# Kernel optimization log

Measured on AMD Instinct MI355X. Metric: run time of the kernel, lower is better.

Reference implementation:

```python
import jax, jax.numpy as jnp
import numpy as np

SQ, B, H = 2048, 1, 4096
NP, HN, MQG = 32, 128, 2          # query heads, head_dim, kv groups
ROT = HN // 2                      # rotary dim = 64 (partial rotary)
NORM = float(np.sqrt(HN))


def apply_rope(x, rope):
    # x: [sq, b, nh, hn]; rope: [sq, 1, ROT//2, 2] (cos, sin)
    sq, b, nh, hn = x.shape
    rot = rope.shape[-2] * 2
    xr, xp = x[..., :rot], x[..., rot:]
    xs = xr.reshape(sq, b, nh, rot // 2, 2)
    rc = rope[:sq].reshape(sq, -1, 1, rot // 2, 2)
    o0 = xs[..., 0] * rc[..., 0] - xs[..., 1] * rc[..., 1]
    o1 = xs[..., 1] * rc[..., 0] + xs[..., 0] * rc[..., 1]
    out = jnp.stack([o0, o1], -1).reshape(sq, b, nh, rot)
    return jnp.concatenate([out, xp], axis=-1)


def setup_inputs() -> dict:
    key = jax.random.key(0)
    k0, k1, k2, k3 = jax.random.split(key, 4)
    qkv_dim = NP * HN + 2 * MQG * HN  # 4608
    hidden_states = jax.random.normal(k0, (SQ, B, H), jnp.float32) * 0.02
    Wqkv = jax.random.normal(k1, (qkv_dim, H), jnp.float32) * 0.02
    bqkv = jax.random.normal(k2, (qkv_dim,), jnp.float32) * 0.02
    Wdense = jax.random.normal(k3, (H, NP * HN), jnp.float32) * 0.02
    # rope cache [sq, 1, ROT//2, 2]
    pos = jnp.arange(SQ, dtype=jnp.float32)
    inv = 1.0 / (10000.0 ** (jnp.arange(0, ROT, 2, dtype=jnp.float32) / ROT))
    ang = pos[:, None] * inv[None, :]
    rotary_pos_emb = jnp.stack([jnp.cos(ang), jnp.sin(ang)], -1)[:, None, :, :]
    # additive causal mask [b, 1, sq, sq]
    causal = jnp.tril(jnp.ones((SQ, SQ), bool))
    attention_mask = jnp.broadcast_to(
        jnp.where(causal, 0.0, -1e9).astype(jnp.float32), (B, 1, SQ, SQ))
    return dict(hidden_states=hidden_states, Wqkv=Wqkv, bqkv=bqkv,
                Wdense=Wdense, rotary_pos_emb=rotary_pos_emb,
                attention_mask=attention_mask)


def reference(hidden_states, Wqkv, bqkv, Wdense, rotary_pos_emb, attention_mask):
    sq, b, _ = hidden_states.shape
    mixed = hidden_states @ Wqkv.T + bqkv            # [sq, b, 4608]
    qd, kvd = NP * HN, MQG * HN
    q = mixed[..., :qd].reshape(sq, b, NP, HN)
    k = mixed[..., qd:qd + kvd].reshape(sq, b, MQG, HN)
    v = mixed[..., qd + kvd:].reshape(sq, b, MQG, HN)
    q = apply_rope(q, rotary_pos_emb)
    k = apply_rope(k, rotary_pos_emb)
    # -> [b, heads, sq, hn]
    q = q.transpose(1, 2, 0, 3)
    k = k.transpose(1, 2, 0, 3)
    v = v.transpose(1, 2, 0, 3)
    # MQA grouping: q [b, g, n_rep, sq, hn]; kv kept at [b, g, sq, hn]
    n_rep = NP // MQG
    qg = q.reshape(b, MQG, n_rep, sq, HN)
    scores = jnp.einsum('bgrqd,bgkd->bgrqk', qg, k) / NORM
    scores = scores + attention_mask[:, None]        # [b,1,1,sq,sq] broadcast
    probs = jax.nn.softmax(scores.astype(jnp.float32), axis=-1).astype(q.dtype)
    ctx = jnp.einsum('bgrqk,bgkd->bgrqd', probs, v)  # [b, g, n_rep, sq, hn]
    ctx = ctx.reshape(b, NP, sq, HN).transpose(0, 2, 1, 3).reshape(b, sq, NP * HN)
    out = ctx @ Wdense.T                             # [b, sq, H]
    return out
```

## Files before the change

kernel.cpp:

```cpp
#include <hip/hip_runtime.h>
#include <stdint.h>

#define SQL 2048
#define HID 4096
#define NHEADS 32
#define HDSZ 128
#define QKVD 4608
#define QDIM 4096

typedef unsigned short u16;
typedef __attribute__((ext_vector_type(8))) short short8;
typedef __attribute__((ext_vector_type(4))) float f32x4;

#define AS1(p) ((__attribute__((address_space(1))) void*)(p))
#define AS3(p) ((__attribute__((address_space(3))) void*)(p))

__device__ __forceinline__ float bf2f(u16 u) {
  return __uint_as_float(((uint32_t)u) << 16);
}
__device__ __forceinline__ u16 f2bf(float f) {
  uint32_t x = __float_as_uint(f);
  x += 0x7fffu + ((x >> 16) & 1u);
  return (u16)(x >> 16);
}

__global__ void k_cvt(const float* __restrict__ in, u16* __restrict__ out, int n8) {
  int i = blockIdx.x * blockDim.x + threadIdx.x;
  int stride = gridDim.x * blockDim.x;
  for (; i < n8; i += stride) {
    const float4* p = reinterpret_cast<const float4*>(in) + (size_t)i * 2;
    float4 a = p[0], b = p[1];
    short8 o;
    o[0] = (short)f2bf(a.x); o[1] = (short)f2bf(a.y);
    o[2] = (short)f2bf(a.z); o[3] = (short)f2bf(a.w);
    o[4] = (short)f2bf(b.x); o[5] = (short)f2bf(b.y);
    o[6] = (short)f2bf(b.z); o[7] = (short)f2bf(b.w);
    reinterpret_cast<short8*>(out)[i] = o;
  }
}

template<int MODE>
__global__ __launch_bounds__(256, 2)
void k_gemm(const u16* __restrict__ A, const u16* __restrict__ B,
            const float* __restrict__ bias,
            u16* __restrict__ qbuf, u16* __restrict__ kbuf, u16* __restrict__ vtbuf,
            float* __restrict__ outf)
{
  __shared__ __align__(16) u16 ldsA[128 * 64];
  __shared__ __align__(16) u16 ldsB[128 * 64];
  const int tid = threadIdx.x;
  const int wid = tid >> 6, lane = tid & 63;
  const int l15 = lane & 15, lg = lane >> 4;
  const int m0 = blockIdx.y * 128, n0 = blockIdx.x * 128;
  const int wr = wid >> 1, wc = wid & 1;

  f32x4 acc[4][4] = {};

  const int srow = lane >> 3;
  const int skb  = (((lane & 7) ^ srow) << 4);
  const size_t rowbytes = (size_t)HID * 2;

  for (int t = 0; t < HID / 64; ++t) {
    __syncthreads();
    const char* Ab = (const char*)A + (size_t)m0 * rowbytes + (size_t)t * 128;
    const char* Bb = (const char*)B + (size_t)n0 * rowbytes + (size_t)t * 128;
#pragma unroll
    for (int i = 0; i < 4; ++i) {
      int seg = i * 4 + wid;
      int row = seg * 8 + srow;
      __builtin_amdgcn_global_load_lds(AS1(Ab + (size_t)row * rowbytes + skb),
                                       AS3(ldsA + seg * 512), 16, 0, 0);
      __builtin_amdgcn_global_load_lds(AS1(Bb + (size_t)row * rowbytes + skb),
                                       AS3(ldsB + seg * 512), 16, 0, 0);
    }
    __syncthreads();
#pragma unroll
    for (int kc = 0; kc < 2; ++kc) {
      short8 af[4], bfr[4];
#pragma unroll
      for (int mi = 0; mi < 4; ++mi) {
        int row = wr * 64 + mi * 16 + l15;
        int kb = (kc * 64 + lg * 16) ^ ((row & 7) << 4);
        af[mi] = *reinterpret_cast<const short8*>((const char*)ldsA + row * 128 + kb);
      }
#pragma unroll
      for (int ni = 0; ni < 4; ++ni) {
        int row = wc * 64 + ni * 16 + l15;
        int kb = (kc * 64 + lg * 16) ^ ((row & 7) << 4);
        bfr[ni] = *reinterpret_cast<const short8*>((const char*)ldsB + row * 128 + kb);
      }
#pragma unroll
      for (int mi = 0; mi < 4; ++mi)
#pragma unroll
        for (int ni = 0; ni < 4; ++ni)
          acc[mi][ni] = __builtin_amdgcn_mfma_f32_16x16x32_bf16(af[mi], bfr[ni], acc[mi][ni], 0, 0, 0);
    }
  }

#pragma unroll
  for (int mi = 0; mi < 4; ++mi) {
#pragma unroll
    for (int ni = 0; ni < 4; ++ni) {
      int row0 = m0 + wr * 64 + mi * 16 + lg * 4;
      int col  = n0 + wc * 64 + ni * 16 + l15;
      if (MODE == 0) {
        float bv = bias[col];
#pragma unroll
        for (int j = 0; j < 4; ++j) {
          float v = acc[mi][ni][j] + bv;
          int r = row0 + j;
          if (col < QDIM) {
            v *= 0.08838834764831845f;
            int hh = col >> 7, d = col & 127;
            qbuf[((size_t)hh * SQL + r) * HDSZ + d] = f2bf(v);
          } else if (col < QDIM + 256) {
            int c2 = col - QDIM; int g = c2 >> 7, d = c2 & 127;
            kbuf[((size_t)g * SQL + r) * HDSZ + d] = f2bf(v);
          } else {
            int c2 = col - QDIM - 256; int g = c2 >> 7, d = c2 & 127;
            vtbuf[((size_t)g * HDSZ + d) * SQL + r] = f2bf(v);
          }
        }
      } else {
#pragma unroll
        for (int j = 0; j < 4; ++j)
          outf[(size_t)(row0 + j) * QDIM + col] = acc[mi][ni][j];
      }
    }
  }
}

__global__ void k_rope(u16* __restrict__ qbuf, u16* __restrict__ kbuf,
                       const float* __restrict__ rope) {
  int idx = blockIdx.x * blockDim.x + threadIdx.x;
  if (idx >= SQL * 34 * 32) return;
  int p = idx & 31;
  int hh = (idx >> 5) % 34;
  int s = idx / (34 * 32);
  float c  = rope[s * 64 + p * 2 + 0];
  float sn = rope[s * 64 + p * 2 + 1];
  u16* base = (hh < 32) ? (qbuf + ((size_t)hh * SQL + s) * HDSZ)
                        : (kbuf + ((size_t)(hh - 32) * SQL + s) * HDSZ);
  u16* pp = base + 2 * p;
  uint32_t packed = *reinterpret_cast<uint32_t*>(pp);
  float x0 = bf2f((u16)(packed & 0xffff));
  float x1 = bf2f((u16)(packed >> 16));
  float o0 = x0 * c - x1 * sn;
  float o1 = x1 * c + x0 * sn;
  *reinterpret_cast<uint32_t*>(pp) = (uint32_t)f2bf(o0) | ((uint32_t)f2bf(o1) << 16);
}

__global__ __launch_bounds__(512, 2)
void k_attn(const u16* __restrict__ qbuf, const u16* __restrict__ kbuf,
            const u16* __restrict__ vtbuf, u16* __restrict__ ctx)
{
  __shared__ __align__(16) u16 KL[2][64 * 128];
  __shared__ __align__(16) u16 VL[2][128 * 64];
  __shared__ uint32_t plw[8][32][36];
  const int tid = threadIdx.x;
  const int wid = tid >> 6, lane = tid & 63;
  const int l15 = lane & 15, lg = lane >> 4;
  const int h = blockIdx.x;
  const int g = h >> 4;
  const int bq = blockIdx.y;
  const int q0 = wid * 256 + bq * 32;
  const int ext = q0 + 32;
  const int NT = (1824 + 32 * bq + 63) >> 6;

  const int cA = tid, cB = tid + 512;
  const int krA = cA >> 4, kiA = (cA & 15) ^ (krA & 7);
  const int krB = cB >> 4, kiB = (cB & 15) ^ (krB & 7);
  const int vrA = cA >> 3, viA = (cA & 7) ^ (vrA & 7);
  const int vrB = cB >> 3, viB = (cB & 7) ^ (vrB & 7);
  const char* kg = (const char*)(kbuf + (size_t)g * SQL * HDSZ);
  const char* vg = (const char*)(vtbuf + (size_t)g * HDSZ * SQL);

#define STAGE(t, b)                                                             \
  do {                                                                          \
    int j0s = (t) * 64;                                                         \
    __builtin_amdgcn_global_load_lds(AS1(kg + (size_t)(j0s + krA) * 256 + (kiA << 4)), \
                                     AS3((char*)KL[b] + cA * 16), 16, 0, 0);    \
    __builtin_amdgcn_global_load_lds(AS1(kg + (size_t)(j0s + krB) * 256 + (kiB << 4)), \
                                     AS3((char*)KL[b] + cB * 16), 16, 0, 0);    \
    __builtin_amdgcn_global_load_lds(AS1(vg + (size_t)vrA * (SQL * 2) + j0s * 2 + (viA << 4)), \
                                     AS3((char*)VL[b] + cA * 16), 16, 0, 0);    \
    __builtin_amdgcn_global_load_lds(AS1(vg + (size_t)vrB * (SQL * 2) + j0s * 2 + (viB << 4)), \
                                     AS3((char*)VL[b] + cB * 16), 16, 0, 0);    \
  } while (0)

  short8 aq[2][4];
#pragma unroll
  for (int rt = 0; rt < 2; ++rt) {
    const u16* qp = qbuf + ((size_t)h * SQL + q0 + rt * 16 + l15) * HDSZ + lg * 8;
#pragma unroll
    for (int kc = 0; kc < 4; ++kc)
      aq[rt][kc] = *reinterpret_cast<const short8*>(qp + kc * 32);
  }
  f32x4 o[2][8] = {};
  float mrow[2], lrow[2];
#pragma unroll
  for (int rt = 0; rt < 2; ++rt) { mrow[rt] = -__builtin_inff(); lrow[rt] = 0.f; }

  STAGE(0, 0);
  __syncthreads();

  for (int i = 0; i < NT; ++i) {
    const int cur = i & 1;
    if (i + 1 < NT) STAGE(i + 1, cur ^ 1);

    const int j0 = i * 64;
    if (j0 < ext) {
      const char* kb0 = (const char*)KL[cur];
      const char* vb0 = (const char*)VL[cur];
      const int swz = (l15 & 7) << 4;

      f32x4 st[2][4] = {};
#pragma unroll
      for (int kc = 0; kc < 4; ++kc) {
        short8 bk4[4];
#pragma unroll
        for (int kt = 0; kt < 4; ++kt) {
          int r = 16 * kt + l15;
          bk4[kt] = *reinterpret_cast<const short8*>(
              kb0 + r * 256 + ((kc * 64 + lg * 16) ^ swz));
        }
        __builtin_amdgcn_s_setprio(1);
#pragma unroll
        for (int rt = 0; rt < 2; ++rt)
#pragma unroll
          for (int kt = 0; kt < 4; ++kt)
            st[rt][kt] = __builtin_amdgcn_mfma_f32_16x16x32_bf16(bk4[kt], aq[rt][kc], st[rt][kt], 0, 0, 0);
        __builtin_amdgcn_s_setprio(0);
      }

      const bool domask = (j0 + 63 > q0);
#pragma unroll
      for (int rt = 0; rt < 2; ++rt) {
        const int q = q0 + rt * 16 + l15;
        float p[4][4];
#pragma unroll
        for (int kt = 0; kt < 4; ++kt)
#pragma unroll
          for (int j = 0; j < 4; ++j) {
            float v = st[rt][kt][j];
            if (domask) {
              int kvi = j0 + kt * 16 + lg * 4 + j;
              v = (kvi > q) ? -1e30f : v;
            }
            p[kt][j] = v;
          }
        float rm = fmaxf(fmaxf(fmaxf(p[0][0], p[0][1]), fmaxf(p[0][2], p[0][3])),
                         fmaxf(fmaxf(p[1][0], p[1][1]), fmaxf(p[1][2], p[1][3])));
        rm = fmaxf(rm, fmaxf(fmaxf(fmaxf(p[2][0], p[2][1]), fmaxf(p[2][2], p[2][3])),
                             fmaxf(fmaxf(p[3][0], p[3][1]), fmaxf(p[3][2], p[3][3]))));
        rm = fmaxf(rm, __shfl_xor(rm, 16));
        rm = fmaxf(rm, __shfl_xor(rm, 32));
        if (!__all(rm <= mrow[rt] + 8.0f)) {
          float mn = fmaxf(mrow[rt], rm);
          float a = __expf(mrow[rt] - mn);
          mrow[rt] = mn;
          lrow[rt] *= a;
          float ar[4];
#pragma unroll
          for (int j = 0; j < 4; ++j) ar[j] = __shfl(a, lg * 4 + j);
#pragma unroll
          for (int df = 0; df < 8; ++df) {
            o[rt][df][0] *= ar[0]; o[rt][df][1] *= ar[1];
            o[rt][df][2] *= ar[2]; o[rt][df][3] *= ar[3];
          }
        }
        float ps = 0.f;
#pragma unroll
        for (int kt = 0; kt < 4; ++kt)
#pragma unroll
          for (int j = 0; j < 4; ++j) {
            p[kt][j] = __expf(p[kt][j] - mrow[rt]);
            ps += p[kt][j];
          }
        ps += __shfl_xor(ps, 16);
        ps += __shfl_xor(ps, 32);
        lrow[rt] += ps;
#pragma unroll
        for (int kt = 0; kt < 4; ++kt)
#pragma unroll
          for (int u = 0; u < 2; ++u) {
            uint32_t W;
            asm("v_cvt_pk_bf16_f32 %0, %1, %2"
                : "=v"(W) : "v"(p[kt][2 * u]), "v"(p[kt][2 * u + 1]));
            plw[wid][rt * 16 + l15][8 * kt + 2 * lg + u] = W;
          }
      }
      asm volatile("s_waitcnt lgkmcnt(0)" ::: "memory");

      short8 ap[2][2];
#pragma unroll
      for (int rt = 0; rt < 2; ++rt)
#pragma unroll
        for (int kc2 = 0; kc2 < 2; ++kc2)
          ap[rt][kc2] = *reinterpret_cast<const short8*>(&plw[wid][rt * 16 + l15][16 * kc2 + 4 * lg]);

      __builtin_amdgcn_s_setprio(1);
#pragma unroll
      for (int df = 0; df < 8; ++df) {
        short8 bv0, bv1;
        int rv = l15 + 16 * df;
#pragma unroll
        for (int kc2 = 0; kc2 < 2; ++kc2) {
          short8 bvv = *reinterpret_cast<const short8*>(
              vb0 + rv * 128 + ((kc2 * 64 + lg * 16) ^ swz));
          if (kc2 == 0) bv0 = bvv; else bv1 = bvv;
        }
#pragma unroll
        for (int rt = 0; rt < 2; ++rt) {
          f32x4 t = o[rt][df];
          t = __builtin_amdgcn_mfma_f32_16x16x32_bf16(ap[rt][0], bv0, t, 0, 0, 0);
          t = __builtin_amdgcn_mfma_f32_16x16x32_bf16(ap[rt][1], bv1, t, 0, 0, 0);
          o[rt][df] = t;
        }
      }
      __builtin_amdgcn_s_setprio(0);
    }
    __syncthreads();
  }

#pragma unroll
  for (int rt = 0; rt < 2; ++rt) {
    float linv[4];
#pragma unroll
    for (int j = 0; j < 4; ++j) linv[j] = 1.0f / __shfl(lrow[rt], lg * 4 + j);
#pragma unroll
    for (int j = 0; j < 4; ++j) {
      int row = q0 + rt * 16 + lg * 4 + j;
      u16* cp = ctx + (size_t)row * QDIM + h * HDSZ;
#pragma unroll
      for (int df = 0; df < 8; ++df)
        cp[df * 16 + l15] = f2bf(o[rt][df][j] * linv[j]);
    }
  }
#undef STAGE
}


extern "C" void kernel_launch(void* const* d_in, const int* in_sizes, int n_in,
                              void* d_out, int out_size, void* d_ws, size_t ws_size,
                              hipStream_t stream) {
  const float* hs     = (const float*)d_in[0];
  const float* wqkv   = (const float*)d_in[1];
  const float* bqkv   = (const float*)d_in[2];
  const float* wdense = (const float*)d_in[3];
  const float* rope   = (const float*)d_in[4];
  char* ws = (char*)d_ws;
  u16* hid_b = (u16*)(ws + 0);
  u16* w_b   = (u16*)(ws + 16777216);
  u16* qb    = (u16*)(ws + 54525952);
  u16* kb    = (u16*)(ws + 71303168);
  u16* vtb   = (u16*)(ws + 72351744);
  u16* ctx   = hid_b;
  float* outf = (float*)d_out;

  k_cvt<<<2048, 256, 0, stream>>>(hs,   hid_b, SQL * HID / 8);
  k_cvt<<<2048, 256, 0, stream>>>(wqkv, w_b,   QKVD * HID / 8);
  k_gemm<0><<<dim3(QKVD / 128, SQL / 128), 256, 0, stream>>>(
      hid_b, w_b, bqkv, qb, kb, vtb, nullptr);
  k_rope<<<(SQL * 34 * 32) / 256, 256, 0, stream>>>(qb, kb, rope);
  k_cvt<<<2048, 256, 0, stream>>>(wdense, w_b, QDIM * HID / 8);
  k_attn<<<dim3(NHEADS, 8), 512, 0, stream>>>(qb, kb, vtb, ctx);
  k_gemm<1><<<dim3(QDIM / 128, SQL / 128), 256, 0, stream>>>(
      ctx, w_b, nullptr, nullptr, nullptr, nullptr, outf);
}
```

Before: 302.3 us.

## Double-buffer GEMM LDS tiles with async prefetch, XCD block swizzle, MFMA priority

Turns the QKV/dense GEMM main loop into a two-stage pipeline. The next K tile is loaded into a second LDS buffer with global_load_lds while MFMAs run on the current one, and synchronisation uses explicit vmcnt waits with raw barriers. Workgroup IDs are remapped so that consecutive tiles land on the same XCD, which improves L2 reuse. s_setprio is raised around the MFMA block. LDS use doubles to 64KB per block, which may reduce occupancy from the two blocks per CU requested in launch bounds.

```diff
diff --git a/kernel.cpp b/kernel.cpp
--- a/kernel.cpp
+++ b/kernel.cpp
@@ -46,12 +46,18 @@
             u16* __restrict__ qbuf, u16* __restrict__ kbuf, u16* __restrict__ vtbuf,
             float* __restrict__ outf)
 {
-  __shared__ __align__(16) u16 ldsA[128 * 64];
-  __shared__ __align__(16) u16 ldsB[128 * 64];
+  __shared__ __align__(16) u16 ldsA[2][128 * 64];
+  __shared__ __align__(16) u16 ldsB[2][128 * 64];
   const int tid = threadIdx.x;
   const int wid = tid >> 6, lane = tid & 63;
   const int l15 = lane & 15, lg = lane >> 4;
-  const int m0 = blockIdx.y * 128, n0 = blockIdx.x * 128;
+
+  const int gridX = gridDim.x;
+  const int nwg = gridX * gridDim.y;
+  const int orig = blockIdx.y * gridX + blockIdx.x;
+  const int cpx = nwg >> 3;
+  const int swz = (orig & 7) * cpx + (orig >> 3);
+  const int m0 = (swz / gridX) * 128, n0 = (swz % gridX) * 128;
   const int wr = wid >> 1, wc = wid & 1;
 
   f32x4 acc[4][4] = {};
@@ -59,21 +65,35 @@
   const int srow = lane >> 3;
   const int skb  = (((lane & 7) ^ srow) << 4);
   const size_t rowbytes = (size_t)HID * 2;
-
-  for (int t = 0; t < HID / 64; ++t) {
-    __syncthreads();
-    const char* Ab = (const char*)A + (size_t)m0 * rowbytes + (size_t)t * 128;
-    const char* Bb = (const char*)B + (size_t)n0 * rowbytes + (size_t)t * 128;
-#pragma unroll
-    for (int i = 0; i < 4; ++i) {
-      int seg = i * 4 + wid;
-      int row = seg * 8 + srow;
-      __builtin_amdgcn_global_load_lds(AS1(Ab + (size_t)row * rowbytes + skb),
-                                       AS3(ldsA + seg * 512), 16, 0, 0);
-      __builtin_amdgcn_global_load_lds(AS1(Bb + (size_t)row * rowbytes + skb),
-                                       AS3(ldsB + seg * 512), 16, 0, 0);
-    }
-    __syncthreads();
+  const int NT = HID / 64;
+
+#define GSTAGE(t, b)                                                            \
+  do {                                                                          \
+    const char* Ab_ = (const char*)A + (size_t)m0 * rowbytes + (size_t)(t) * 128; \
+    const char* Bb_ = (const char*)B + (size_t)n0 * rowbytes + (size_t)(t) * 128; \
+    _Pragma("unroll")                                                           \
+    for (int i_ = 0; i_ < 4; ++i_) {                                            \
+      int seg_ = i_ * 4 + wid;                                                  \
+      int row_ = seg_ * 8 + srow;                                               \
+      __builtin_amdgcn_global_load_lds(AS1(Ab_ + (size_t)row_ * rowbytes + skb),\
+                                       AS3(ldsA[b] + seg_ * 512), 16, 0, 0);    \
+      __builtin_amdgcn_global_load_lds(AS1(Bb_ + (size_t)row_ * rowbytes + skb),\
+                                       AS3(ldsB[b] + seg_ * 512), 16, 0, 0);    \
+    }                                                                           \
+  } while (0)
+
+  GSTAGE(0, 0);
+
+  for (int t = 0; t < NT; ++t) {
+    const int cur = t & 1;
+    if (t + 1 < NT) {
+      GSTAGE(t + 1, cur ^ 1);
+      asm volatile("s_waitcnt vmcnt(8)" ::: "memory");
+    } else {
+      asm volatile("s_waitcnt vmcnt(0)" ::: "memory");
+    }
+    __builtin_amdgcn_s_barrier();
+
 #pragma unroll
     for (int kc = 0; kc < 2; ++kc) {
       short8 af[4], bfr[4];
@@ -81,21 +101,26 @@
       for (int mi = 0; mi < 4; ++mi) {
         int row = wr * 64 + mi * 16 + l15;
         int kb = (kc * 64 + lg * 16) ^ ((row & 7) << 4);
-        af[mi] = *reinterpret_cast<const short8*>((const char*)ldsA + row * 128 + kb);
+        af[mi] = *reinterpret_cast<const short8*>((const char*)ldsA[cur] + row * 128 + kb);
       }
 #pragma unroll
       for (int ni = 0; ni < 4; ++ni) {
         int row = wc * 64 + ni * 16 + l15;
         int kb = (kc * 64 + lg * 16) ^ ((row & 7) << 4);
-        bfr[ni] = *reinterpret_cast<const short8*>((const char*)ldsB + row * 128 + kb);
-      }
+        bfr[ni] = *reinterpret_cast<const short8*>((const char*)ldsB[cur] + row * 128 + kb);
+      }
+      __builtin_amdgcn_s_setprio(1);
 #pragma unroll
       for (int mi = 0; mi < 4; ++mi)
 #pragma unroll
         for (int ni = 0; ni < 4; ++ni)
           acc[mi][ni] = __builtin_amdgcn_mfma_f32_16x16x32_bf16(af[mi], bfr[ni], acc[mi][ni], 0, 0, 0);
-    }
-  }
+      __builtin_amdgcn_s_setprio(0);
+    }
+    asm volatile("" ::: "memory");
+    __builtin_amdgcn_s_barrier();
+  }
+#undef GSTAGE
 
 #pragma unroll
   for (int mi = 0; mi < 4; ++mi) {
```

After: 356.1 us. 1.18x slower.

## Replace output projection GEMM with triple-buffered async-LDS pipelined kernel

Applied to the files above, without the earlier changes.

Splits the templated GEMM into a QKV-specific kernel and a new dense-projection kernel. The new kernel uses 128x256 tiles with 8 waves, a three-stage LDS ring filled via direct global-to-LDS loads two tiles ahead, and interleaves sub-tile LDS reads, prefetch issue, and MFMA bursts with barriers and priority hints. It aims to hide global load latency and raise MFMA utilization for the largest GEMM. In exchange it uses much more LDS, which limits occupancy, and its manual vmcnt bookkeeping makes the ordering fragile.

```diff
diff --git a/kernel.cpp b/kernel.cpp
--- a/kernel.cpp
+++ b/kernel.cpp
@@ -39,12 +39,10 @@
   }
 }
 
-template<int MODE>
 __global__ __launch_bounds__(256, 2)
-void k_gemm(const u16* __restrict__ A, const u16* __restrict__ B,
-            const float* __restrict__ bias,
-            u16* __restrict__ qbuf, u16* __restrict__ kbuf, u16* __restrict__ vtbuf,
-            float* __restrict__ outf)
+void k_gemm1(const u16* __restrict__ A, const u16* __restrict__ B,
+             const float* __restrict__ bias,
+             u16* __restrict__ qbuf, u16* __restrict__ kbuf, u16* __restrict__ vtbuf)
 {
   __shared__ __align__(16) u16 ldsA[128 * 64];
   __shared__ __align__(16) u16 ldsB[128 * 64];
@@ -103,29 +101,141 @@
     for (int ni = 0; ni < 4; ++ni) {
       int row0 = m0 + wr * 64 + mi * 16 + lg * 4;
       int col  = n0 + wc * 64 + ni * 16 + l15;
-      if (MODE == 0) {
-        float bv = bias[col];
-#pragma unroll
-        for (int j = 0; j < 4; ++j) {
-          float v = acc[mi][ni][j] + bv;
-          int r = row0 + j;
-          if (col < QDIM) {
-            v *= 0.08838834764831845f;
-            int hh = col >> 7, d = col & 127;
-            qbuf[((size_t)hh * SQL + r) * HDSZ + d] = f2bf(v);
-          } else if (col < QDIM + 256) {
-            int c2 = col - QDIM; int g = c2 >> 7, d = c2 & 127;
-            kbuf[((size_t)g * SQL + r) * HDSZ + d] = f2bf(v);
-          } else {
-            int c2 = col - QDIM - 256; int g = c2 >> 7, d = c2 & 127;
-            vtbuf[((size_t)g * HDSZ + d) * SQL + r] = f2bf(v);
-          }
+      float bv = bias[col];
+#pragma unroll
+      for (int j = 0; j < 4; ++j) {
+        float v = acc[mi][ni][j] + bv;
+        int r = row0 + j;
+        if (col < QDIM) {
+          v *= 0.08838834764831845f;
+          int hh = col >> 7, d = col & 127;
+          qbuf[((size_t)hh * SQL + r) * HDSZ + d] = f2bf(v);
+        } else if (col < QDIM + 256) {
+          int c2 = col - QDIM; int g = c2 >> 7, d = c2 & 127;
+          kbuf[((size_t)g * SQL + r) * HDSZ + d] = f2bf(v);
+        } else {
+          int c2 = col - QDIM - 256; int g = c2 >> 7, d = c2 & 127;
+          vtbuf[((size_t)g * HDSZ + d) * SQL + r] = f2bf(v);
         }
-      } else {
-#pragma unroll
-        for (int j = 0; j < 4; ++j)
-          outf[(size_t)(row0 + j) * QDIM + col] = acc[mi][ni][j];
-      }
+      }
+    }
+  }
+}
+
+__global__ __launch_bounds__(512, 2)
+void k_gemm2(const u16* __restrict__ A, const u16* __restrict__ B,
+             float* __restrict__ outf)
+{
+  __shared__ __align__(16) u16 ldsA[3][128 * 64];
+  __shared__ __align__(16) u16 ldsB[3][256 * 64];
+  const int tid = threadIdx.x;
+  const int wid = tid >> 6, lane = tid & 63;
+  const int l15 = lane & 15, lg = lane >> 4;
+  const int m0 = blockIdx.y * 128, n0 = blockIdx.x * 256;
+  const int wm = wid >> 2, wn = wid & 3;
+  const int rsw = (l15 & 7) << 4;
+  const size_t rb = (size_t)HID * 2;
+  const int NT = HID / 64;
+
+  f32x4 acc[4][4] = {};
+
+#define STG_A(t, b) do {                                                        \
+    _Pragma("unroll")                                                           \
+    for (int u_ = 0; u_ < 2; ++u_) {                                            \
+      int ch_ = tid + u_ * 512;                                                 \
+      int r_ = ch_ >> 3, s_ = ch_ & 7, g_ = s_ ^ (r_ & 7);                      \
+      __builtin_amdgcn_global_load_lds(                                         \
+        AS1((const char*)A + (size_t)(m0 + r_) * rb + (size_t)(t) * 128 + g_ * 16), \
+        AS3((char*)ldsA[b] + ch_ * 16), 16, 0, 0);                              \
+    } } while (0)
+#define STG_B(t, b, u0) do {                                                    \
+    _Pragma("unroll")                                                           \
+    for (int u_ = (u0); u_ < (u0) + 2; ++u_) {                                  \
+      int ch_ = tid + u_ * 512;                                                 \
+      int r_ = ch_ >> 3, s_ = ch_ & 7, g_ = s_ ^ (r_ & 7);                      \
+      __builtin_amdgcn_global_load_lds(                                         \
+        AS1((const char*)B + (size_t)(n0 + r_) * rb + (size_t)(t) * 128 + g_ * 16), \
+        AS3((char*)ldsB[b] + ch_ * 16), 16, 0, 0);                              \
+    } } while (0)
+#define LDA_(bf_, mi, kc) (*reinterpret_cast<const short8*>(                    \
+    (const char*)ldsA[bf_] + (wm * 64 + (mi) * 16 + l15) * 128 +                \
+    (((kc) * 64 + lg * 16) ^ rsw)))
+#define LDB_(bf_, ni, kc) (*reinterpret_cast<const short8*>(                    \
+    (const char*)ldsB[bf_] + (wn * 64 + (ni) * 16 + l15) * 128 +                \
+    (((kc) * 64 + lg * 16) ^ rsw)))
+#define MF8(mA, mB) do {                                                        \
+    _Pragma("unroll")                                                           \
+    for (int ni_ = 0; ni_ < 4; ++ni_) {                                         \
+      acc[mA][ni_] = __builtin_amdgcn_mfma_f32_16x16x32_bf16(af0, bf[ni_], acc[mA][ni_], 0, 0, 0); \
+      acc[mB][ni_] = __builtin_amdgcn_mfma_f32_16x16x32_bf16(af1, bf[ni_], acc[mB][ni_], 0, 0, 0); \
+    } } while (0)
+
+  STG_A(0, 0); STG_B(0, 0, 0); STG_B(0, 0, 2);
+  STG_A(1, 1); STG_B(1, 1, 0); STG_B(1, 1, 2);
+  asm volatile("s_waitcnt vmcnt(6)" ::: "memory");
+  __builtin_amdgcn_s_barrier();
+
+  for (int t = 0; t < NT; ++t) {
+    const int cur = t % 3, nb = (t + 2) % 3;
+    const bool st = (t + 2) < NT;
+    short8 af0, af1, bf[4];
+
+    af0 = LDA_(cur, 0, 0); af1 = LDA_(cur, 1, 0);
+    bf[0] = LDB_(cur, 0, 0); bf[1] = LDB_(cur, 1, 0);
+    bf[2] = LDB_(cur, 2, 0); bf[3] = LDB_(cur, 3, 0);
+    if (st) STG_A(t + 2, nb);
+    __builtin_amdgcn_s_barrier();
+    __builtin_amdgcn_sched_barrier(0);
+    __builtin_amdgcn_s_setprio(1);
+    MF8(0, 1);
+    __builtin_amdgcn_s_setprio(0);
+    __builtin_amdgcn_s_barrier();
+
+    af0 = LDA_(cur, 2, 0); af1 = LDA_(cur, 3, 0);
+    if (st) STG_B(t + 2, nb, 0);
+    __builtin_amdgcn_s_barrier();
+    __builtin_amdgcn_sched_barrier(0);
+    __builtin_amdgcn_s_setprio(1);
+    MF8(2, 3);
+    __builtin_amdgcn_s_setprio(0);
+    __builtin_amdgcn_s_barrier();
+
+    af0 = LDA_(cur, 0, 1); af1 = LDA_(cur, 1, 1);
+    bf[0] = LDB_(cur, 0, 1); bf[1] = LDB_(cur, 1, 1);
+    bf[2] = LDB_(cur, 2, 1); bf[3] = LDB_(cur, 3, 1);
+    if (st) STG_B(t + 2, nb, 2);
+    __builtin_amdgcn_s_barrier();
+    __builtin_amdgcn_sched_barrier(0);
+    __builtin_amdgcn_s_setprio(1);
+    MF8(0, 1);
+    __builtin_amdgcn_s_setprio(0);
+    __builtin_amdgcn_s_barrier();
+
+    af0 = LDA_(cur, 2, 1); af1 = LDA_(cur, 3, 1);
+    __builtin_amdgcn_s_barrier();
+    __builtin_amdgcn_sched_barrier(0);
+    __builtin_amdgcn_s_setprio(1);
+    MF8(2, 3);
+    __builtin_amdgcn_s_setprio(0);
+    if (st) asm volatile("s_waitcnt vmcnt(6)" ::: "memory");
+    else    asm volatile("s_waitcnt vmcnt(0)" ::: "memory");
+    __builtin_amdgcn_s_barrier();
+  }
+#undef STG_A
+#undef STG_B
+#undef LDA_
+#undef LDB_
+#undef MF8
+
+#pragma unroll
+  for (int mi = 0; mi < 4; ++mi) {
+#pragma unroll
+    for (int ni = 0; ni < 4; ++ni) {
+      int row0 = m0 + wm * 64 + mi * 16 + lg * 4;
+      int col  = n0 + wn * 64 + ni * 16 + l15;
+#pragma unroll
+      for (int j = 0; j < 4; ++j)
+        outf[(size_t)(row0 + j) * QDIM + col] = acc[mi][ni][j];
     }
   }
 }
@@ -360,11 +470,10 @@
 
   k_cvt<<<2048, 256, 0, stream>>>(hs,   hid_b, SQL * HID / 8);
   k_cvt<<<2048, 256, 0, stream>>>(wqkv, w_b,   QKVD * HID / 8);
-  k_gemm<0><<<dim3(QKVD / 128, SQL / 128), 256, 0, stream>>>(
-      hid_b, w_b, bqkv, qb, kb, vtb, nullptr);
+  k_gemm1<<<dim3(QKVD / 128, SQL / 128), 256, 0, stream>>>(
+      hid_b, w_b, bqkv, qb, kb, vtb);
   k_rope<<<(SQL * 34 * 32) / 256, 256, 0, stream>>>(qb, kb, rope);
   k_cvt<<<2048, 256, 0, stream>>>(wdense, w_b, QDIM * HID / 8);
   k_attn<<<dim3(NHEADS, 8), 512, 0, stream>>>(qb, kb, vtb, ctx);
-  k_gemm<1><<<dim3(QDIM / 128, SQL / 128), 256, 0, stream>>>(
-      ctx, w_b, nullptr, nullptr, nullptr, nullptr, outf);
-}
+  k_gemm2<<<dim3(QDIM / 256, SQL / 128), 512, 0, stream>>>(ctx, w_b, outf);
+}
```

Result: slower. 323.3 us (+6.9%).
